# Optimization experiments

Hardware: AMD Instinct MI355X
Metric: run time of the kernel (lower is better)

The kernel has to match this reference:

```python
import jax, jax.numpy as jnp
import numpy as np

HIDDEN = 4096
NHEADS = 32
HEAD_DIM = HIDDEN // NHEADS
ROPE_BASE = 10000.0
VISION_TOKEN_TYPE = 1


def setup_inputs() -> dict:
    key = jax.random.key(0)
    ks = jax.random.split(key, 8)
    B, L = 2, 2048
    hidden_states = jax.random.normal(ks[0], (B, L, HIDDEN), dtype=jnp.float32)
    token_type_ids = jax.random.randint(ks[1], (B, L), 0, 2)
    position_ids = jnp.broadcast_to(jnp.arange(L), (B, L))
    attention_mask = jnp.zeros((B, 1, L, L), dtype=jnp.float32)
    s = 1.0 / np.sqrt(HIDDEN)
    w_v_qkv = jax.random.normal(ks[2], (3 * HIDDEN, HIDDEN), dtype=jnp.float32) * s
    w_l_qkv = jax.random.normal(ks[3], (3 * HIDDEN, HIDDEN), dtype=jnp.float32) * s
    w_v_dense = jax.random.normal(ks[4], (HIDDEN, HIDDEN), dtype=jnp.float32) * s
    w_l_dense = jax.random.normal(ks[5], (HIDDEN, HIDDEN), dtype=jnp.float32) * s
    return {
        'hidden_states': hidden_states,
        'token_type_ids': token_type_ids,
        'position_ids': position_ids,
        'attention_mask': attention_mask,
        'w_v_qkv': w_v_qkv,
        'w_l_qkv': w_l_qkv,
        'w_v_dense': w_v_dense,
        'w_l_dense': w_l_dense,
    }


def _rotate_half(x):
    x1, x2 = jnp.split(x, 2, axis=-1)
    return jnp.concatenate((-x2, x1), axis=-1)


def _rope_tables(max_pos, dtype):
    inv_freq = 1.0 / (ROPE_BASE ** (jnp.arange(0, HEAD_DIM, 2, dtype=jnp.float32) / HEAD_DIM))
    t = jnp.arange(max_pos, dtype=jnp.float32)
    freqs = jnp.einsum('i,j->ij', t, inv_freq)
    emb = jnp.concatenate((freqs, freqs), axis=-1)  # [max_pos, head_dim]
    return jnp.cos(emb).astype(dtype), jnp.sin(emb).astype(dtype)


def reference(hidden_states, token_type_ids, position_ids, attention_mask,
              w_v_qkv, w_l_qkv, w_v_dense, w_l_dense):
    B, L, H = hidden_states.shape
    # expert masks: vision token if both it and the next token are vision type
    tt = token_type_ids
    vm = jnp.zeros_like(tt, dtype=bool)
    vm = vm.at[:, :-1].set((tt[:, :-1] == VISION_TOKEN_TYPE) & (tt[:, 1:] == VISION_TOKEN_TYPE))
    vmf = vm[..., None].astype(hidden_states.dtype)  # [B, L, 1]

    # routed QKV: compute both experts, select per token (same math as scatter)
    qkv_v = jnp.einsum('blh,oh->blo', hidden_states, w_v_qkv)
    qkv_l = jnp.einsum('blh,oh->blo', hidden_states, w_l_qkv)
    mixed = vmf * qkv_v + (1.0 - vmf) * qkv_l  # [B, L, 3H]

    q, k, v = jnp.split(mixed, 3, axis=-1)
    def to_bhld(x):
        return x.reshape(B, L, NHEADS, HEAD_DIM).transpose(0, 2, 1, 3)
    q, k, v = to_bhld(q), to_bhld(k), to_bhld(v)

    # RoPE gathered by position_ids
    cos_t, sin_t = _rope_tables(L, hidden_states.dtype)
    cos = cos_t[position_ids][:, None, :, :]  # [B, 1, L, head_dim]
    sin = sin_t[position_ids][:, None, :, :]
    q = q * cos + _rotate_half(q) * sin
    k = k * cos + _rotate_half(k) * sin

    # full (non-causal) SDPA since attention_mask is all zeros
    scale = 1.0 / jnp.sqrt(jnp.asarray(HEAD_DIM, dtype=q.dtype))
    scores = jnp.einsum('bhqd,bhkd->bhqk', q * scale, k)
    probs = jax.nn.softmax(scores, axis=-1)
    ctx = jnp.einsum('bhqk,bhkd->bhqd', probs, v)
    ctx = ctx.transpose(0, 2, 1, 3).reshape(B, L, H)

    # routed output dense
    out_v = jnp.einsum('blh,oh->blo', ctx, w_v_dense)
    out_l = jnp.einsum('blh,oh->blo', ctx, w_l_dense)
    attn_output = vmf * out_v + (1.0 - vmf) * out_l
    return attn_output
```

## Files before the change

kernel.cpp:

```cpp
#include <hip/hip_runtime.h>
#include <hip/hip_bf16.h>
#include <math.h>


typedef __bf16 bf16_t;
typedef __bf16 bf16x8 __attribute__((ext_vector_type(8)));
typedef __bf16 bf16x4 __attribute__((ext_vector_type(4)));
typedef float  f32x4  __attribute__((ext_vector_type(4)));

#define BSZ   2
#define SEQ   2048
#define NTOK  (BSZ * SEQ)
#define MPAD  (NTOK + 128)
#define HID   4096
#define NH    32
#define HD    128
#define QKV3  (3 * HID)

__device__ __forceinline__ void gld_lds16(const bf16_t* g, bf16_t* l) {
  __builtin_amdgcn_global_load_lds(
      (const __attribute__((address_space(1))) unsigned int*)g,
      (__attribute__((address_space(3))) unsigned int*)l, 16, 0, 0);
}

__global__ __launch_bounds__(256) void castk(const float* __restrict__ in,
                                             bf16_t* __restrict__ out,
                                             long long n) {
  long long i = ((long long)blockIdx.x * 256 + threadIdx.x) * 4;
  if (i >= n) return;
  float4 v = *(const float4*)(in + i);
  bf16x4 o;
  o[0] = (bf16_t)v.x; o[1] = (bf16_t)v.y; o[2] = (bf16_t)v.z; o[3] = (bf16_t)v.w;
  *(bf16x4*)(out + i) = o;
}

__global__ __launch_bounds__(256) void cast_gather(const float* __restrict__ in,
                                                   bf16_t* __restrict__ out,
                                                   const int* __restrict__ ginv) {
  long long i = ((long long)blockIdx.x * 256 + threadIdx.x) * 4;
  int token = (int)(i >> 12);
  int col = (int)(i & 4095);
  float4 v = *(const float4*)(in + i);
  bf16x4 o;
  o[0] = (bf16_t)v.x; o[1] = (bf16_t)v.y; o[2] = (bf16_t)v.z; o[3] = (bf16_t)v.w;
  *(bf16x4*)(out + (size_t)ginv[token] * HID + col) = o;
}

__global__ __launch_bounds__(1024) void scan_kernel(const int* __restrict__ tt,
                                                    int* __restrict__ perm_src,
                                                    int* __restrict__ ginv,
                                                    int* __restrict__ meta) {
  __shared__ int sums[1024];
  const int t = threadIdx.x;
  for (int i = t; i < MPAD; i += 1024) perm_src[i] = -1;
  int v[4], s = 0;
#pragma unroll
  for (int j = 0; j < 4; j++) {
    int tok = t * 4 + j;
    int l = tok & (SEQ - 1);
    int vis = (l < SEQ - 1) && (tt[tok] == 1) && (tt[tok + 1] == 1);
    v[j] = vis; s += vis;
  }
  sums[t] = s;
  __syncthreads();
  for (int off = 1; off < 1024; off <<= 1) {
    int x = sums[t];
    int y = (t >= off) ? sums[t - off] : 0;
    __syncthreads();
    sums[t] = x + y;
    __syncthreads();
  }
  const int nv = sums[1023];
  const int nvpad = (nv + 127) & ~127;
  int pv = sums[t] - s;
#pragma unroll
  for (int j = 0; j < 4; j++) {
    int tok = t * 4 + j;
    int dst;
    if (v[j]) { dst = pv; pv++; }
    else      { dst = nvpad + (tok - pv); }
    perm_src[dst] = tok;
    ginv[tok] = dst;
  }
  if (t == 0) meta[0] = nvpad >> 7;
}

template <int OUT_F32>
__global__ __launch_bounds__(256) void gemm_routed(
    const bf16_t* __restrict__ A, const bf16_t* __restrict__ Bv,
    const bf16_t* __restrict__ Bl, void* __restrict__ Cout, int N, int K,
    const int* __restrict__ perm_src, const int* __restrict__ meta) {
  __shared__ bf16_t As[128 * 32];
  __shared__ bf16_t Bs[128 * 32];
  const int tid = threadIdx.x;
  const int bm = blockIdx.x, bn = blockIdx.y;
  const bf16_t* __restrict__ B = (bm < meta[0]) ? Bv : Bl;
  const int wv = tid >> 6, lane = tid & 63, lr = lane & 15, quad = lane >> 4;
  const int wm = (wv >> 1) * 64, wn = (wv & 1) * 64;

  const int r0 = tid >> 2;
  const int c0 = ((tid & 3) ^ ((tid >> 3) & 3)) * 8;
  const bf16_t* a0 = A + (size_t)(bm * 128 + r0) * K + c0;
  const bf16_t* a1 = A + (size_t)(bm * 128 + r0 + 64) * K + c0;
  const bf16_t* b0 = B + (size_t)(bn * 128 + r0) * K + c0;
  const bf16_t* b1 = B + (size_t)(bn * 128 + r0 + 64) * K + c0;
  bf16_t* asD0 = &As[(tid & ~63) * 8];
  bf16_t* asD1 = &As[(256 + (tid & ~63)) * 8];
  bf16_t* bsD0 = &Bs[(tid & ~63) * 8];
  bf16_t* bsD1 = &Bs[(256 + (tid & ~63)) * 8];

  const int pp = (quad ^ ((lr >> 1) & 3)) * 8;

  f32x4 acc[4][4] = {};

  for (int kt = 0; kt < K; kt += 32) {
    gld_lds16(a0 + kt, asD0);
    gld_lds16(a1 + kt, asD1);
    gld_lds16(b0 + kt, bsD0);
    gld_lds16(b1 + kt, bsD1);
    __syncthreads();
    bf16x8 af[4], bfr[4];
#pragma unroll
    for (int i = 0; i < 4; i++)
      af[i] = *(const bf16x8*)&As[(wm + i * 16 + lr) * 32 + pp];
#pragma unroll
    for (int j = 0; j < 4; j++)
      bfr[j] = *(const bf16x8*)&Bs[(wn + j * 16 + lr) * 32 + pp];
#pragma unroll
    for (int i = 0; i < 4; i++)
#pragma unroll
      for (int j = 0; j < 4; j++)
        acc[i][j] = __builtin_amdgcn_mfma_f32_16x16x32_bf16(af[i], bfr[j],
                                                            acc[i][j], 0, 0, 0);
    __syncthreads();
  }

#pragma unroll
  for (int i = 0; i < 4; i++) {
#pragma unroll
    for (int r = 0; r < 4; r++) {
      int rowg = bm * 128 + wm + i * 16 + quad * 4 + r;
      int src = perm_src[rowg];
      if (src < 0) continue;
      size_t rowoff = (size_t)src * N + bn * 128 + wn + lr;
#pragma unroll
      for (int j = 0; j < 4; j++) {
        if (OUT_F32)
          ((float*)Cout)[rowoff + j * 16] = acc[i][j][r];
        else
          ((bf16_t*)Cout)[rowoff + j * 16] = (bf16_t)acc[i][j][r];
      }
    }
  }
}

__global__ __launch_bounds__(256) void rope_split(
    const bf16_t* __restrict__ mixed, const int* __restrict__ pos_ids,
    bf16_t* __restrict__ qbuf, bf16_t* __restrict__ kbuf) {
  int idx = blockIdx.x * 256 + threadIdx.x;
  int d2 = idx & 63;
  int h = (idx >> 6) & 31;
  int token = idx >> 11;
  int b = token >> 11;
  int l = token & (SEQ - 1);
  int pos = pos_ids[token];
  float inv = expf((float)d2 * -0.14391156831212787f);
  float ang = (float)pos * inv;
  float c = cosf(ang), s = sinf(ang);

  const bf16_t* row = mixed + (size_t)token * QKV3;
  float q1 = (float)row[h * HD + d2];
  float q2 = (float)row[h * HD + d2 + 64];
  float k1 = (float)row[HID + h * HD + d2];
  float k2 = (float)row[HID + h * HD + d2 + 64];

  size_t base = ((size_t)(b * NH + h) * SEQ + l) * HD;
  qbuf[base + d2]      = (bf16_t)(q1 * c - q2 * s);
  qbuf[base + d2 + 64] = (bf16_t)(q2 * c + q1 * s);
  kbuf[base + d2]      = (bf16_t)(k1 * c - k2 * s);
  kbuf[base + d2 + 64] = (bf16_t)(k2 * c + k1 * s);
}

__global__ __launch_bounds__(256) void vtrans(const bf16_t* __restrict__ mixed,
                                              bf16_t* __restrict__ vbuf) {
  __shared__ bf16_t tile[64][130];
  const int bh = blockIdx.x;
  const int lt = blockIdx.y;
  const int b = bh >> 5, h = bh & 31;
  const int tid = threadIdx.x;
#pragma unroll
  for (int i = 0; i < 32; i++) {
    int s = i * 256 + tid;
    int l = s >> 7, d = s & 127;
    size_t token = (size_t)b * SEQ + lt * 64 + l;
    tile[l][d] = mixed[token * QKV3 + 2 * HID + h * HD + d];
  }
  __syncthreads();
#pragma unroll
  for (int i = 0; i < 32; i++) {
    int s = i * 256 + tid;
    int d = s >> 6, l = s & 63;
    vbuf[((size_t)bh * HD + d) * SEQ + lt * 64 + l] = tile[l][d];
  }
}

__global__ __launch_bounds__(256) void attn_fwd(
    const bf16_t* __restrict__ qb, const bf16_t* __restrict__ kb,
    const bf16_t* __restrict__ vb, bf16_t* __restrict__ ctxg,
    const int* __restrict__ ginv) {
  __shared__ bf16_t Ks[64 * 128];
  __shared__ bf16_t Vs[128 * 64];
  __shared__ bf16_t Ps[4 * 32 * 64];
  const int bh = blockIdx.x, qt = blockIdx.y;
  const int b = bh >> 5, h = bh & 31;
  const int tid = threadIdx.x;
  const int wv = tid >> 6, lane = tid & 63, lr = lane & 15, quad = lane >> 4;
  const int qrow0 = qt * 128 + wv * 32;

  const bf16_t* qbase = qb + (size_t)bh * SEQ * HD;
  const bf16_t* kbase = kb + (size_t)bh * SEQ * HD;
  const bf16_t* vbase = vb + (size_t)bh * HD * SEQ;

  bf16x8 qf[2][4];
#pragma unroll
  for (int i = 0; i < 2; i++)
#pragma unroll
    for (int ds = 0; ds < 4; ds++)
      qf[i][ds] = *(const bf16x8*)(qbase + (size_t)(qrow0 + i * 16 + lr) * HD +
                                   ds * 32 + quad * 8);

  f32x4 O[2][8] = {};
  float mst[2][4], lst[2][4];
#pragma unroll
  for (int i = 0; i < 2; i++)
#pragma unroll
    for (int r = 0; r < 4; r++) { mst[i][r] = -1e30f; lst[i][r] = 0.f; }

  const float scale = 0.08838834764831845f;
  const int l7 = lr & 7;

  for (int kt = 0; kt < SEQ / 64; kt++) {
    const bf16_t* ksrc = kbase + (size_t)kt * 64 * HD;
    const bf16_t* vsrc = vbase + kt * 64;
#pragma unroll
    for (int inst = 0; inst < 4; inst++) {
      int s = inst * 256 + tid;
      int krow = s >> 4, kg = (s & 15) ^ (krow & 7);
      gld_lds16(ksrc + (size_t)krow * HD + kg * 8,
                &Ks[(inst * 256 + (tid & ~63)) * 8]);
      int vrow = s >> 3, vg = (s & 7) ^ (vrow & 7);
      gld_lds16(vsrc + (size_t)vrow * SEQ + vg * 8,
                &Vs[(inst * 256 + (tid & ~63)) * 8]);
    }
    __syncthreads();

    f32x4 S[2][4] = {};
#pragma unroll
    for (int ds = 0; ds < 4; ds++) {
      bf16x8 kf[4];
#pragma unroll
      for (int n = 0; n < 4; n++)
        kf[n] = *(const bf16x8*)&Ks[(n * 16 + lr) * HD +
                                    ((ds * 4 + quad) ^ l7) * 8];
#pragma unroll
      for (int i = 0; i < 2; i++)
#pragma unroll
        for (int n = 0; n < 4; n++)
          S[i][n] = __builtin_amdgcn_mfma_f32_16x16x32_bf16(qf[i][ds], kf[n],
                                                            S[i][n], 0, 0, 0);
    }

    bf16_t* pw = &Ps[wv * 32 * 64];
#pragma unroll
    for (int i = 0; i < 2; i++) {
      float rmax[4];
#pragma unroll
      for (int r = 0; r < 4; r++) {
        float m = -1e30f;
#pragma unroll
        for (int n = 0; n < 4; n++) {
          S[i][n][r] *= scale;
          m = fmaxf(m, S[i][n][r]);
        }
#pragma unroll
        for (int off = 1; off < 16; off <<= 1)
          m = fmaxf(m, __shfl_xor(m, off, 64));
        rmax[r] = m;
      }
#pragma unroll
      for (int r = 0; r < 4; r++) {
        float mnew = fmaxf(mst[i][r], rmax[r]);
        float alpha = __expf(mst[i][r] - mnew);
        mst[i][r] = mnew;
        float rsum = 0.f;
#pragma unroll
        for (int n = 0; n < 4; n++) {
          float p = __expf(S[i][n][r] - mnew);
          S[i][n][r] = p;
          rsum += p;
        }
#pragma unroll
        for (int off = 1; off < 16; off <<= 1) rsum += __shfl_xor(rsum, off, 64);
        lst[i][r] = lst[i][r] * alpha + rsum;
#pragma unroll
        for (int n = 0; n < 8; n++) O[i][n][r] *= alpha;
        int row = i * 16 + quad * 4 + r;
#pragma unroll
        for (int n = 0; n < 4; n++) {
          int e = n * 16 + lr;
          pw[row * 64 + (((e >> 3) ^ (row & 7)) * 8) + (e & 7)] =
              (bf16_t)S[i][n][r];
        }
      }
    }

#pragma unroll
    for (int ks = 0; ks < 2; ks++) {
      bf16x8 pf[2], vf[8];
#pragma unroll
      for (int i = 0; i < 2; i++)
        pf[i] = *(const bf16x8*)&pw[(i * 16 + lr) * 64 +
                                    ((ks * 4 + quad) ^ l7) * 8];
#pragma unroll
      for (int n = 0; n < 8; n++)
        vf[n] = *(const bf16x8*)&Vs[(n * 16 + lr) * 64 +
                                    ((ks * 4 + quad) ^ l7) * 8];
#pragma unroll
      for (int i = 0; i < 2; i++)
#pragma unroll
        for (int n = 0; n < 8; n++)
          O[i][n] = __builtin_amdgcn_mfma_f32_16x16x32_bf16(pf[i], vf[n],
                                                            O[i][n], 0, 0, 0);
    }
    __syncthreads();
  }

#pragma unroll
  for (int i = 0; i < 2; i++)
#pragma unroll
    for (int r = 0; r < 4; r++) {
      float inv = 1.0f / lst[i][r];
      int tok = b * SEQ + qt * 128 + wv * 32 + i * 16 + quad * 4 + r;
      size_t dst = (size_t)ginv[tok] * HID + h * HD;
#pragma unroll
      for (int n = 0; n < 8; n++)
        ctxg[dst + n * 16 + lr] = (bf16_t)(O[i][n][r] * inv);
    }
}

extern "C" void kernel_launch(void* const* d_in, const int* in_sizes, int n_in,
                              void* d_out, int out_size, void* d_ws, size_t ws_size,
                              hipStream_t stream) {
  const float* hs  = (const float*)d_in[0];
  const int*   tt  = (const int*)d_in[1];
  const int*   pos = (const int*)d_in[2];
  const float* wvq = (const float*)d_in[4];
  const float* wlq = (const float*)d_in[5];
  const float* wvd = (const float*)d_in[6];
  const float* wld = (const float*)d_in[7];
  float* out = (float*)d_out;

  char* ws = (char*)d_ws;
  size_t off = 0;
  auto alloc = [&](size_t bytes) -> char* {
    char* p = ws + off;
    off += (bytes + 255) & ~(size_t)255;
    return p;
  };
  bf16_t* hsg   = (bf16_t*)alloc((size_t)MPAD * HID * 2);
  bf16_t* wvqb  = (bf16_t*)alloc((size_t)QKV3 * HID * 2);
  bf16_t* wlqb  = (bf16_t*)alloc((size_t)QKV3 * HID * 2);
  bf16_t* wvdb  = (bf16_t*)alloc((size_t)HID * HID * 2);
  bf16_t* wldb  = (bf16_t*)alloc((size_t)HID * HID * 2);
  bf16_t* mixed = (bf16_t*)alloc((size_t)NTOK * QKV3 * 2);
  bf16_t* qbuf  = (bf16_t*)alloc((size_t)NTOK * HID * 2);
  bf16_t* kbuf  = (bf16_t*)alloc((size_t)NTOK * HID * 2);
  bf16_t* vbuf  = (bf16_t*)alloc((size_t)NTOK * HID * 2);
  int* perm_src = (int*)alloc((size_t)MPAD * 4);
  int* ginv     = (int*)alloc((size_t)NTOK * 4);
  int* meta     = (int*)alloc(256);
  bf16_t* ctxg  = mixed;

  scan_kernel<<<dim3(1), dim3(1024), 0, stream>>>(tt, perm_src, ginv, meta);

  cast_gather<<<dim3(NTOK * HID / 1024), dim3(256), 0, stream>>>(hs, hsg, ginv);
  auto cast = [&](const float* in, bf16_t* o, long long n) {
    castk<<<dim3((unsigned)((n + 1023) / 1024)), dim3(256), 0, stream>>>(in, o, n);
  };
  cast(wvq, wvqb, (long long)QKV3 * HID);
  cast(wlq, wlqb, (long long)QKV3 * HID);
  cast(wvd, wvdb, (long long)HID * HID);
  cast(wld, wldb, (long long)HID * HID);

  gemm_routed<0><<<dim3(MPAD / 128, QKV3 / 128), dim3(256), 0, stream>>>(
      hsg, wvqb, wlqb, mixed, QKV3, HID, perm_src, meta);

  rope_split<<<dim3((NTOK * NH * 64) / 256), dim3(256), 0, stream>>>(mixed, pos,
                                                                     qbuf, kbuf);
  vtrans<<<dim3(BSZ * NH, SEQ / 64), dim3(256), 0, stream>>>(mixed, vbuf);

  attn_fwd<<<dim3(BSZ * NH, SEQ / 128), dim3(256), 0, stream>>>(qbuf, kbuf, vbuf,
                                                                ctxg, ginv);

  gemm_routed<1><<<dim3(MPAD / 128, HID / 128), dim3(256), 0, stream>>>(
      ctxg, wvdb, wldb, out, HID, HID, perm_src, meta);
}
```

Before: 2.166 ms.

## Double-buffer routed GEMM LDS tiles and remap workgroups across XCDs

```diff
diff --git a/kernel.cpp b/kernel.cpp
--- a/kernel.cpp
+++ b/kernel.cpp
@@ -16,6 +16,7 @@
 #define NH    32
 #define HD    128
 #define QKV3  (3 * HID)
+#define GM    (MPAD / 128)
 
 __device__ __forceinline__ void gld_lds16(const bf16_t* g, bf16_t* l) {
   __builtin_amdgcn_global_load_lds(
@@ -85,15 +86,53 @@
   if (t == 0) meta[0] = nvpad >> 7;
 }
 
+#define GEMM_STAGE(AS, BS, kt)                              \
+  do {                                                      \
+    gld_lds16(a0 + (kt), &AS[(tid & ~63) * 8]);             \
+    gld_lds16(a1 + (kt), &AS[(256 + (tid & ~63)) * 8]);     \
+    gld_lds16(b0 + (kt), &BS[(tid & ~63) * 8]);             \
+    gld_lds16(b1 + (kt), &BS[(256 + (tid & ~63)) * 8]);     \
+  } while (0)
+
+#define GEMM_COMPUTE(AS, BS)                                                 \
+  do {                                                                       \
+    bf16x8 af[4], bfr[4];                                                    \
+    _Pragma("unroll") for (int i = 0; i < 4; i++)                            \
+        af[i] = *(const bf16x8*)&AS[(wm + i * 16 + lr) * 32 + pp];           \
+    _Pragma("unroll") for (int j = 0; j < 4; j++)                            \
+        bfr[j] = *(const bf16x8*)&BS[(wn + j * 16 + lr) * 32 + pp];          \
+    __builtin_amdgcn_s_setprio(1);                                          \
+    _Pragma("unroll") for (int i = 0; i < 4; i++)                            \
+        _Pragma("unroll") for (int j = 0; j < 4; j++)                        \
+            acc[i][j] = __builtin_amdgcn_mfma_f32_16x16x32_bf16(             \
+                af[i], bfr[j], acc[i][j], 0, 0, 0);                          \
+    __builtin_amdgcn_s_setprio(0);                                          \
+  } while (0)
+
+#define GEMM_BOUNDARY                                       \
+  do {                                                      \
+    asm volatile("s_waitcnt vmcnt(0)" ::: "memory");        \
+    __builtin_amdgcn_s_barrier();                           \
+  } while (0)
+
 template <int OUT_F32>
 __global__ __launch_bounds__(256) void gemm_routed(
     const bf16_t* __restrict__ A, const bf16_t* __restrict__ Bv,
     const bf16_t* __restrict__ Bl, void* __restrict__ Cout, int N, int K,
     const int* __restrict__ perm_src, const int* __restrict__ meta) {
-  __shared__ bf16_t As[128 * 32];
-  __shared__ bf16_t Bs[128 * 32];
+  __shared__ bf16_t As0[128 * 32];
+  __shared__ bf16_t Bs0[128 * 32];
+  __shared__ bf16_t As1[128 * 32];
+  __shared__ bf16_t Bs1[128 * 32];
   const int tid = threadIdx.x;
-  const int bm = blockIdx.x, bn = blockIdx.y;
+
+  const int nwg = gridDim.x;
+  const int q = nwg >> 3, r = nwg & 7;
+  const int xcd = blockIdx.x & 7, pos = blockIdx.x >> 3;
+  const int wgid = (xcd < r ? xcd * (q + 1) : r * (q + 1) + (xcd - r) * q) + pos;
+  const int bm = wgid % GM;
+  const int bn = wgid / GM;
+
   const bf16_t* __restrict__ B = (bm < meta[0]) ? Bv : Bl;
   const int wv = tid >> 6, lane = tid & 63, lr = lane & 15, quad = lane >> 4;
   const int wm = (wv >> 1) * 64, wn = (wv & 1) * 64;
@@ -104,51 +143,42 @@
   const bf16_t* a1 = A + (size_t)(bm * 128 + r0 + 64) * K + c0;
   const bf16_t* b0 = B + (size_t)(bn * 128 + r0) * K + c0;
   const bf16_t* b1 = B + (size_t)(bn * 128 + r0 + 64) * K + c0;
-  bf16_t* asD0 = &As[(tid & ~63) * 8];
-  bf16_t* asD1 = &As[(256 + (tid & ~63)) * 8];
-  bf16_t* bsD0 = &Bs[(tid & ~63) * 8];
-  bf16_t* bsD1 = &Bs[(256 + (tid & ~63)) * 8];
 
   const int pp = (quad ^ ((lr >> 1) & 3)) * 8;
 
   f32x4 acc[4][4] = {};
 
-  for (int kt = 0; kt < K; kt += 32) {
-    gld_lds16(a0 + kt, asD0);
-    gld_lds16(a1 + kt, asD1);
-    gld_lds16(b0 + kt, bsD0);
-    gld_lds16(b1 + kt, bsD1);
-    __syncthreads();
-    bf16x8 af[4], bfr[4];
-#pragma unroll
-    for (int i = 0; i < 4; i++)
-      af[i] = *(const bf16x8*)&As[(wm + i * 16 + lr) * 32 + pp];
-#pragma unroll
-    for (int j = 0; j < 4; j++)
-      bfr[j] = *(const bf16x8*)&Bs[(wn + j * 16 + lr) * 32 + pp];
-#pragma unroll
-    for (int i = 0; i < 4; i++)
-#pragma unroll
-      for (int j = 0; j < 4; j++)
-        acc[i][j] = __builtin_amdgcn_mfma_f32_16x16x32_bf16(af[i], bfr[j],
-                                                            acc[i][j], 0, 0, 0);
-    __syncthreads();
-  }
+  GEMM_STAGE(As0, Bs0, 0);
+  GEMM_BOUNDARY;
+  int kt = 32;
+  for (int s = 0; s < (K >> 5) - 2; s += 2) {
+    GEMM_STAGE(As1, Bs1, kt);
+    GEMM_COMPUTE(As0, Bs0);
+    GEMM_BOUNDARY;
+    GEMM_STAGE(As0, Bs0, kt + 32);
+    GEMM_COMPUTE(As1, Bs1);
+    GEMM_BOUNDARY;
+    kt += 64;
+  }
+  GEMM_STAGE(As1, Bs1, kt);
+  GEMM_COMPUTE(As0, Bs0);
+  GEMM_BOUNDARY;
+  GEMM_COMPUTE(As1, Bs1);
 
 #pragma unroll
   for (int i = 0; i < 4; i++) {
 #pragma unroll
-    for (int r = 0; r < 4; r++) {
-      int rowg = bm * 128 + wm + i * 16 + quad * 4 + r;
+    for (int rr = 0; rr < 4; rr++) {
+      int rowg = bm * 128 + wm + i * 16 + quad * 4 + rr;
       int src = perm_src[rowg];
       if (src < 0) continue;
       size_t rowoff = (size_t)src * N + bn * 128 + wn + lr;
 #pragma unroll
       for (int j = 0; j < 4; j++) {
         if (OUT_F32)
-          ((float*)Cout)[rowoff + j * 16] = acc[i][j][r];
+          ((float*)Cout)[rowoff + j * 16] = acc[i][j][rr];
         else
-          ((bf16_t*)Cout)[rowoff + j * 16] = (bf16_t)acc[i][j][r];
+          ((bf16_t*)Cout)[rowoff + j * 16] = (bf16_t)acc[i][j][rr];
       }
     }
   }
@@ -392,7 +422,7 @@
   cast(wvd, wvdb, (long long)HID * HID);
   cast(wld, wldb, (long long)HID * HID);
 
-  gemm_routed<0><<<dim3(MPAD / 128, QKV3 / 128), dim3(256), 0, stream>>>(
+  gemm_routed<0><<<dim3(GM * (QKV3 / 128)), dim3(256), 0, stream>>>(
       hsg, wvqb, wlqb, mixed, QKV3, HID, perm_src, meta);
 
   rope_split<<<dim3((NTOK * NH * 64) / 256), dim3(256), 0, stream>>>(mixed, pos,
@@ -402,6 +432,6 @@
   attn_fwd<<<dim3(BSZ * NH, SEQ / 128), dim3(256), 0, stream>>>(qbuf, kbuf, vbuf,
                                                                 ctxg, ginv);
 
-  gemm_routed<1><<<dim3(MPAD / 128, HID / 128), dim3(256), 0, stream>>>(
+  gemm_routed<1><<<dim3(GM * (HID / 128)), dim3(256), 0, stream>>>(
       ctxg, wvdb, wldb, out, HID, HID, perm_src, meta);
 }
```

After: 1.936 ms. -10.6%, faster.

## Rewrite routed GEMM with 256x256 tiles, double-buffered LDS pipeline, XCD remap

Applied to the files above, without the earlier changes.

```diff
diff --git a/kernel.cpp b/kernel.cpp
--- a/kernel.cpp
+++ b/kernel.cpp
@@ -11,11 +11,12 @@
 #define BSZ   2
 #define SEQ   2048
 #define NTOK  (BSZ * SEQ)
-#define MPAD  (NTOK + 128)
+#define MPAD  (NTOK + 256)
 #define HID   4096
 #define NH    32
 #define HD    128
 #define QKV3  (3 * HID)
+#define GM    (MPAD / 256)
 
 __device__ __forceinline__ void gld_lds16(const bf16_t* g, bf16_t* l) {
   __builtin_amdgcn_global_load_lds(
@@ -71,7 +72,7 @@
     __syncthreads();
   }
   const int nv = sums[1023];
-  const int nvpad = (nv + 127) & ~127;
+  const int nvpad = (nv + 255) & ~255;
   int pv = sums[t] - s;
 #pragma unroll
   for (int j = 0; j < 4; j++) {
@@ -82,73 +83,149 @@
     perm_src[dst] = tok;
     ginv[tok] = dst;
   }
-  if (t == 0) meta[0] = nvpad >> 7;
-}
+  if (t == 0) meta[0] = nvpad >> 8;
+}
+
+
+#define BAR                                  \
+  do {                                       \
+    asm volatile("" ::: "memory");           \
+    __builtin_amdgcn_s_barrier();            \
+    asm volatile("" ::: "memory");           \
+  } while (0)
+
+#define VMW(N) asm volatile("s_waitcnt vmcnt(" #N ")" ::: "memory")
+
+#define LDA(BUF, mh)                                                       \
+  _Pragma("unroll") for (int m_ = 0; m_ < 4; m_++)                         \
+    _Pragma("unroll") for (int kk_ = 0; kk_ < 2; kk_++)                    \
+      af[m_][kk_] = *(const bf16x8*)((const char*)As[BUF] +                \
+          (size_t)((wr * 128 + (mh) * 64 + m_ * 16 + lr) * 128 +           \
+                   (((kk_ * 4 + quad) ^ l7) * 16)));
+
+#define LDB(BUF)                                                           \
+  _Pragma("unroll") for (int n_ = 0; n_ < 4; n_++)                         \
+    _Pragma("unroll") for (int kk_ = 0; kk_ < 2; kk_++)                    \
+      bfr[n_][kk_] = *(const bf16x8*)((const char*)Bs[BUF] +               \
+          (size_t)((wc * 64 + n_ * 16 + lr) * 128 +                        \
+                   (((kk_ * 4 + quad) ^ l7) * 16)));
+
+#define MMQ(mh, nh)                                                        \
+  __builtin_amdgcn_s_setprio(1);                                           \
+  _Pragma("unroll") for (int kk_ = 0; kk_ < 2; kk_++)                      \
+    _Pragma("unroll") for (int m_ = 0; m_ < 4; m_++)                       \
+      _Pragma("unroll") for (int n_ = 0; n_ < 2; n_++)                     \
+        acc[(mh) * 4 + m_][(nh) * 2 + n_] =                                \
+            __builtin_amdgcn_mfma_f32_16x16x32_bf16(                       \
+                af[m_][kk_], bfr[(nh) * 2 + n_][kk_],                      \
+                acc[(mh) * 4 + m_][(nh) * 2 + n_], 0, 0, 0);               \
+  __builtin_amdgcn_s_setprio(0);
 
 template <int OUT_F32>
-__global__ __launch_bounds__(256) void gemm_routed(
+__global__ __launch_bounds__(512, 2) void gemm_routed(
     const bf16_t* __restrict__ A, const bf16_t* __restrict__ Bv,
     const bf16_t* __restrict__ Bl, void* __restrict__ Cout, int N, int K,
     const int* __restrict__ perm_src, const int* __restrict__ meta) {
-  __shared__ bf16_t As[128 * 32];
-  __shared__ bf16_t Bs[128 * 32];
+  __shared__ bf16_t As[2][256 * 64];
+  __shared__ bf16_t Bs[2][256 * 64];
   const int tid = threadIdx.x;
-  const int bm = blockIdx.x, bn = blockIdx.y;
-  const bf16_t* __restrict__ B = (bm < meta[0]) ? Bv : Bl;
-  const int wv = tid >> 6, lane = tid & 63, lr = lane & 15, quad = lane >> 4;
-  const int wm = (wv >> 1) * 64, wn = (wv & 1) * 64;
-
-  const int r0 = tid >> 2;
-  const int c0 = ((tid & 3) ^ ((tid >> 3) & 3)) * 8;
-  const bf16_t* a0 = A + (size_t)(bm * 128 + r0) * K + c0;
-  const bf16_t* a1 = A + (size_t)(bm * 128 + r0 + 64) * K + c0;
-  const bf16_t* b0 = B + (size_t)(bn * 128 + r0) * K + c0;
-  const bf16_t* b1 = B + (size_t)(bn * 128 + r0 + 64) * K + c0;
-  bf16_t* asD0 = &As[(tid & ~63) * 8];
-  bf16_t* asD1 = &As[(256 + (tid & ~63)) * 8];
-  bf16_t* bsD0 = &Bs[(tid & ~63) * 8];
-  bf16_t* bsD1 = &Bs[(256 + (tid & ~63)) * 8];
-
-  const int pp = (quad ^ ((lr >> 1) & 3)) * 8;
-
-  f32x4 acc[4][4] = {};
-
-  for (int kt = 0; kt < K; kt += 32) {
-    gld_lds16(a0 + kt, asD0);
-    gld_lds16(a1 + kt, asD1);
-    gld_lds16(b0 + kt, bsD0);
-    gld_lds16(b1 + kt, bsD1);
-    __syncthreads();
-    bf16x8 af[4], bfr[4];
-#pragma unroll
-    for (int i = 0; i < 4; i++)
-      af[i] = *(const bf16x8*)&As[(wm + i * 16 + lr) * 32 + pp];
-#pragma unroll
-    for (int j = 0; j < 4; j++)
-      bfr[j] = *(const bf16x8*)&Bs[(wn + j * 16 + lr) * 32 + pp];
-#pragma unroll
-    for (int i = 0; i < 4; i++)
-#pragma unroll
-      for (int j = 0; j < 4; j++)
-        acc[i][j] = __builtin_amdgcn_mfma_f32_16x16x32_bf16(af[i], bfr[j],
-                                                            acc[i][j], 0, 0, 0);
-    __syncthreads();
-  }
-
-#pragma unroll
-  for (int i = 0; i < 4; i++) {
-#pragma unroll
-    for (int r = 0; r < 4; r++) {
-      int rowg = bm * 128 + wm + i * 16 + quad * 4 + r;
+  const int wv = tid >> 6, lane = tid & 63;
+  const int lr = lane & 15, quad = lane >> 4, l7 = lr & 7;
+  const int wr = wv >> 2, wc = wv & 3;
+
+  const int nwg = gridDim.x;
+  const int q = nwg >> 3, r = nwg & 7;
+  const int xcd = blockIdx.x & 7, pos = blockIdx.x >> 3;
+  const int wgid = (xcd < r ? xcd * (q + 1) : r * (q + 1) + (xcd - r) * q) + pos;
+  const int bm = wgid % GM;
+  const int bn = wgid / GM;
+  const bf16_t* __restrict__ Bp = (bm < meta[0]) ? Bv : Bl;
+
+  const bf16_t* Ab = A + (size_t)(bm * 256) * K;
+  const bf16_t* Bb = Bp + (size_t)(bn * 256) * K;
+
+  const int srow = lane >> 3;
+  const int schunk = (lane & 7) ^ srow;
+  auto stage = [&](bf16_t* ldsbase, const bf16_t* gbase) {
+#pragma unroll
+    for (int j = 0; j < 2; j++) {
+      int s = wv * 2 + j;
+      gld_lds16(gbase + (size_t)(s * 8 + srow) * K + schunk * 8,
+                ldsbase + s * 512);
+    }
+  };
+
+  f32x4 acc[8][4] = {};
+  bf16x8 af[4][2], bfr[4][2];
+
+  const size_t KH = 128 * (size_t)K;
+
+  stage(&Bs[0][0],    Bb);
+  stage(&Bs[0][8192], Bb + KH);
+  stage(&As[0][0],    Ab);
+  stage(&As[0][8192], Ab + KH);
+  stage(&Bs[1][0],    Bb + 64);
+  stage(&Bs[1][8192], Bb + KH + 64);
+  stage(&As[1][0],    Ab + 64);
+  VMW(6);
+  BAR;
+
+  for (int i = 0; i < (K >> 7) - 1; ++i) {
+    const size_t c1 = (size_t)(2 * i + 1) * 64;
+    const size_t c2 = c1 + 64, c3 = c1 + 128;
+    LDA(0, 0); LDB(0);
+    stage(&As[1][8192], Ab + KH + c1);
+    BAR; MMQ(0, 0); BAR;
+    stage(&Bs[0][0], Bb + c2);
+    BAR; MMQ(0, 1); BAR;
+    LDA(0, 1);
+    stage(&Bs[0][8192], Bb + KH + c2);
+    BAR; MMQ(1, 1); BAR;
+    stage(&As[0][0], Ab + c2);
+    BAR; MMQ(1, 0); VMW(6); BAR;
+    LDA(1, 0); LDB(1);
+    stage(&As[0][8192], Ab + KH + c2);
+    BAR; MMQ(0, 0); BAR;
+    stage(&Bs[1][0], Bb + c3);
+    BAR; MMQ(0, 1); BAR;
+    LDA(1, 1);
+    stage(&Bs[1][8192], Bb + KH + c3);
+    BAR; MMQ(1, 1); BAR;
+    stage(&As[1][0], Ab + c3);
+    BAR; MMQ(1, 0); VMW(6); BAR;
+  }
+
+  {
+    const size_t cl = (size_t)((K >> 6) - 1) * 64;
+    LDA(0, 0); LDB(0);
+    stage(&As[1][8192], Ab + KH + cl);
+    BAR; MMQ(0, 0); BAR;
+    BAR; MMQ(0, 1); BAR;
+    LDA(0, 1);
+    BAR; MMQ(1, 1); BAR;
+    BAR; MMQ(1, 0); VMW(0); BAR;
+    LDA(1, 0); LDB(1);
+    BAR; MMQ(0, 0); BAR;
+    BAR; MMQ(0, 1); BAR;
+    LDA(1, 1);
+    BAR; MMQ(1, 1); BAR;
+    BAR; MMQ(1, 0);
+  }
+
+#pragma unroll
+  for (int m = 0; m < 8; m++) {
+#pragma unroll
+    for (int rr = 0; rr < 4; rr++) {
+      int rowg = bm * 256 + wr * 128 + m * 16 + quad * 4 + rr;
       int src = perm_src[rowg];
       if (src < 0) continue;
-      size_t rowoff = (size_t)src * N + bn * 128 + wn + lr;
-#pragma unroll
-      for (int j = 0; j < 4; j++) {
+      size_t rowoff = (size_t)src * N + bn * 256 + wc * 64 + lr;
+#pragma unroll
+      for (int n = 0; n < 4; n++) {
         if (OUT_F32)
-          ((float*)Cout)[rowoff + j * 16] = acc[i][j][r];
+          ((float*)Cout)[rowoff + n * 16] = acc[m][n][rr];
         else
-          ((bf16_t*)Cout)[rowoff + j * 16] = (bf16_t)acc[i][j][r];
+          ((bf16_t*)Cout)[rowoff + n * 16] = (bf16_t)acc[m][n][rr];
       }
     }
   }
@@ -392,7 +469,7 @@
   cast(wvd, wvdb, (long long)HID * HID);
   cast(wld, wldb, (long long)HID * HID);
 
-  gemm_routed<0><<<dim3(MPAD / 128, QKV3 / 128), dim3(256), 0, stream>>>(
+  gemm_routed<0><<<dim3(GM * (QKV3 / 256)), dim3(512), 0, stream>>>(
       hsg, wvqb, wlqb, mixed, QKV3, HID, perm_src, meta);
 
   rope_split<<<dim3((NTOK * NH * 64) / 256), dim3(256), 0, stream>>>(mixed, pos,
@@ -402,6 +479,6 @@
   attn_fwd<<<dim3(BSZ * NH, SEQ / 128), dim3(256), 0, stream>>>(qbuf, kbuf, vbuf,
                                                                 ctxg, ginv);
 
-  gemm_routed<1><<<dim3(MPAD / 128, HID / 128), dim3(256), 0, stream>>>(
+  gemm_routed<1><<<dim3(GM * (HID / 256)), dim3(512), 0, stream>>>(
       ctxg, wvdb, wldb, out, HID, HID, perm_src, meta);
 }
```

New measurement: 1.836 ms. 15.2% less time.
